# Optimization experiments

Measured on AMD Instinct MI355X. Metric: run time of the kernel, lower is better.

The kernel has to match this reference:

```python
import jax, jax.numpy as jnp
import numpy as np

D_K, D_MODEL, NUM_HEADS = 64, 1024, 16


def _xavier(key, shape):
    # xavier_uniform over last two dims (fan_in=shape[-2], fan_out=shape[-1])
    fan_in, fan_out = shape[-2], shape[-1]
    limit = float(np.sqrt(6.0 / (fan_in + fan_out)))
    return jax.random.uniform(key, shape, jnp.float32, -limit, limit)


def setup_inputs() -> dict:
    key = jax.random.key(0)
    kx, kq, kk, kv, ko = jax.random.split(key, 5)
    x = jax.random.normal(kx, (2, 2048, D_MODEL), dtype=jnp.float32)
    w_q = _xavier(kq, (NUM_HEADS, D_MODEL, D_K))
    w_k = _xavier(kk, (NUM_HEADS, D_MODEL, D_K))
    w_v = _xavier(kv, (NUM_HEADS, D_MODEL, D_K))
    w_o = _xavier(ko, (NUM_HEADS * D_K, D_MODEL))
    return {"x": x, "w_q": w_q, "w_k": w_k, "w_v": w_v, "w_o": w_o}


def reference(x, w_q, w_k, w_v, w_o):
    scale = 1.0 / jnp.sqrt(jnp.asarray(D_K, dtype=jnp.float32))
    q = jnp.einsum('bsd,hdk->bhsk', x, w_q)
    k = jnp.einsum('bsd,hdk->bhsk', x, w_k)
    v = jnp.einsum('bsd,hdk->bhsk', x, w_v)
    scores = jnp.einsum('bhqk,bhmk->bhqm', q, k) * scale  # [B,H,S,S]
    weights = jax.nn.softmax(scores, axis=-1)
    z = jnp.einsum('bhqm,bhmk->bhqk', weights, v)
    b, h, s, dk = z.shape
    z = jnp.transpose(z, (0, 2, 1, 3)).reshape(b, s, h * dk)
    z = jnp.einsum('bse,ed->bsd', z, w_o)
    return x + z  # dropout_prob=0.0 (eval): identity
```

## Files before the change

### kernel.cpp

```cpp
#include <hip/hip_runtime.h>
#include <hip/hip_bf16.h>
#include <stdint.h>

typedef float    f32x4  __attribute__((ext_vector_type(4)));
typedef __bf16   bf16x8 __attribute__((ext_vector_type(8)));
typedef __bf16   bf16x2 __attribute__((ext_vector_type(2)));
typedef uint16_t u16;

#define NHEADS 16
#define DKV    64
#define DMODEL 1024
#define BATCH  2
#define SEQ    2048
#define ROWS   4096

#define EXP2F(x) __builtin_amdgcn_exp2f(x)

__device__ __forceinline__ u16 f2bf(float f) {
  __bf16 h = (__bf16)f;
  union { __bf16 h; u16 u; } c; c.h = h; return c.u;
}
__device__ __forceinline__ uint32_t pk2(float a, float b) {
  union { bf16x2 v; uint32_t u; } c;
  c.v = (bf16x2){(__bf16)a, (__bf16)b};
  return c.u;
}

__device__ __forceinline__ void gload16(const void* g, void* l) {
  __builtin_amdgcn_global_load_lds(
      (const __attribute__((address_space(1))) uint32_t*)g,
      (__attribute__((address_space(3))) uint32_t*)l, 16, 0, 0);
}

__device__ __forceinline__ f32x4 mfma16(bf16x8 a, bf16x8 b, f32x4 c) {
  return __builtin_amdgcn_mfma_f32_16x16x32_bf16(a, b, c, 0, 0, 0);
}

__global__ void prep_kernel(const float* __restrict__ x, u16* __restrict__ xb,
                            const float* __restrict__ wq, const float* __restrict__ wk,
                            const float* __restrict__ wv, const float* __restrict__ wo,
                            u16* __restrict__ wt, u16* __restrict__ wot) {
  int blk = blockIdx.x, tid = threadIdx.x;
  if (blk < 2048) {
    int i = blk * 256 + tid;
    const float4* p = (const float4*)(x + (size_t)i * 8);
    float4 a = p[0], b = p[1];
    uint32_t o0 = pk2(a.x, a.y), o1 = pk2(a.z, a.w);
    uint32_t o2 = pk2(b.x, b.y), o3 = pk2(b.z, b.w);
    uint4 pk = make_uint4(o0, o1, o2, o3);
    *(uint4*)(xb + (size_t)i * 8) = pk;
    return;
  }
  __shared__ float t[64][65];
  int wblk = blk - 2048;
  const float* src; u16* dst; int sld, dld;
  if (wblk < 768) {
    int p = wblk >> 8, rem = wblk & 255;
    int h = rem >> 4, dt = rem & 15;
    const float* w = (p == 0) ? wq : (p == 1) ? wk : wv;
    src = w + ((size_t)h * 1024 + dt * 64) * 64;   sld = 64;
    dst = wt + ((size_t)(p * 1024 + h * 64)) * 1024 + dt * 64; dld = 1024;
  } else {
    int t2 = wblk - 768, rt = t2 >> 4, ct = t2 & 15;
    src = wo + (size_t)(rt * 64) * 1024 + ct * 64;  sld = 1024;
    dst = wot + (size_t)(ct * 64) * 1024 + rt * 64; dld = 1024;
  }
#pragma unroll
  for (int i = 0; i < 16; i++) {
    int e = tid + i * 256, r = e >> 6, c = e & 63;
    t[r][c] = src[(size_t)r * sld + c];
  }
  __syncthreads();
#pragma unroll
  for (int i = 0; i < 16; i++) {
    int e = tid + i * 256, r = e >> 6, c = e & 63;
    dst[(size_t)r * dld + c] = f2bf(t[c][r]);
  }
}

__global__ __launch_bounds__(256) void qkv_gemm(
    const u16* __restrict__ xb, const u16* __restrict__ wt,
    u16* __restrict__ qout, u16* __restrict__ kout, u16* __restrict__ vout) {
  __shared__ __align__(16) u16 As[128 * 64];
  __shared__ __align__(16) u16 Bs[128 * 64];
  int tid = threadIdx.x, l = tid & 63, w = tid >> 6;
  int cpx = gridDim.x >> 3;
  int bid = (blockIdx.x & 7) * cpx + (blockIdx.x >> 3);
  bool vpath = bid >= 512;
  const u16 *A, *Bt; int m0, n0;
  if (!vpath) { A = xb; Bt = wt; m0 = (bid >> 4) * 128; n0 = (bid & 15) * 128; }
  else { int b2 = bid - 512; A = wt + (size_t)2048 * 1024; Bt = xb;
         m0 = (b2 >> 5) * 128; n0 = (b2 & 31) * 128; }
  int wm = (w >> 1) * 64, wn = (w & 1) * 64;
  int cg = l >> 4, cl = l & 15;
  int scb = (l & 7) ^ (l >> 3);
  int swz = (cl & 7) << 4;

  f32x4 acc[4][4];
#pragma unroll
  for (int i = 0; i < 4; i++)
#pragma unroll
    for (int j = 0; j < 4; j++) acc[i][j] = (f32x4){0.f, 0.f, 0.f, 0.f};

  for (int k0 = 0; k0 < 1024; k0 += 64) {
    __syncthreads();
    const u16* ga = A  + (size_t)(m0 + w * 32 + (l >> 3)) * 1024 + k0 + scb * 8;
    const u16* gb = Bt + (size_t)(n0 + w * 32 + (l >> 3)) * 1024 + k0 + scb * 8;
#pragma unroll
    for (int j = 0; j < 4; j++) {
      gload16(ga + (size_t)(j * 8) * 1024, &As[(w * 32 + j * 8) * 64]);
      gload16(gb + (size_t)(j * 8) * 1024, &Bs[(w * 32 + j * 8) * 64]);
    }
    __syncthreads();

    bf16x8 af[4][2], bfr[4][2];
#pragma unroll
    for (int mi = 0; mi < 4; mi++) {
      const char* ap = (const char*)&As[(wm + mi * 16 + cl) * 64];
      af[mi][0] = *(const bf16x8*)(ap + ((cg * 16)      ^ swz));
      af[mi][1] = *(const bf16x8*)(ap + ((64 + cg * 16) ^ swz));
    }
#pragma unroll
    for (int ni = 0; ni < 4; ni++) {
      const char* bp = (const char*)&Bs[(wn + ni * 16 + cl) * 64];
      bfr[ni][0] = *(const bf16x8*)(bp + ((cg * 16)      ^ swz));
      bfr[ni][1] = *(const bf16x8*)(bp + ((64 + cg * 16) ^ swz));
    }
#pragma unroll
    for (int mi = 0; mi < 4; mi++)
#pragma unroll
      for (int ni = 0; ni < 4; ni++) {
        acc[mi][ni] = mfma16(af[mi][0], bfr[ni][0], acc[mi][ni]);
        acc[mi][ni] = mfma16(af[mi][1], bfr[ni][1], acc[mi][ni]);
      }
  }

#pragma unroll
  for (int mi = 0; mi < 4; mi++)
#pragma unroll
    for (int ni = 0; ni < 4; ni++) {
      int nbase = n0 + wn + ni * 16 + cl;
#pragma unroll
      for (int r = 0; r < 4; r++) {
        int m = m0 + wm + mi * 16 + cg * 4 + r;
        float v = acc[mi][ni][r];
        if (!vpath) {
          int p = nbase >> 10, hh = (nbase >> 6) & 15, dk = nbase & 63;
          int b = m >> 11, s = m & 2047;
          size_t o = ((size_t)(b * 16 + hh) * 2048 + s) * 64 + dk;
          if (p == 0) qout[o] = f2bf(v * 0.18033688f);
          else        kout[o] = f2bf(v);
        } else {
          vout[(size_t)m * 4096 + nbase] = f2bf(v);
        }
      }
    }
}

__global__ __launch_bounds__(256) void out_gemm(
    const u16* __restrict__ A, const u16* __restrict__ Bt,
    const float* __restrict__ xres, float* __restrict__ fout) {
  __shared__ __align__(16) u16 As[128 * 64];
  __shared__ __align__(16) u16 Bs[64 * 64];
  int tid = threadIdx.x, l = tid & 63, w = tid >> 6;
  int cpx = gridDim.x >> 3;
  int bid = (blockIdx.x & 7) * cpx + (blockIdx.x >> 3);
  int m0 = (bid >> 4) * 128, n0 = (bid & 15) * 64;
  int wm = (w >> 1) * 64, wn = (w & 1) * 32;
  int cg = l >> 4, cl = l & 15;
  int scb = (l & 7) ^ (l >> 3);
  int swz = (cl & 7) << 4;

  f32x4 acc[4][2];
#pragma unroll
  for (int i = 0; i < 4; i++)
#pragma unroll
    for (int j = 0; j < 2; j++) acc[i][j] = (f32x4){0.f, 0.f, 0.f, 0.f};

  for (int k0 = 0; k0 < 1024; k0 += 64) {
    __syncthreads();
    const u16* ga = A  + (size_t)(m0 + w * 32 + (l >> 3)) * 1024 + k0 + scb * 8;
    const u16* gb = Bt + (size_t)(n0 + w * 16 + (l >> 3)) * 1024 + k0 + scb * 8;
#pragma unroll
    for (int j = 0; j < 4; j++)
      gload16(ga + (size_t)(j * 8) * 1024, &As[(w * 32 + j * 8) * 64]);
#pragma unroll
    for (int j = 0; j < 2; j++)
      gload16(gb + (size_t)(j * 8) * 1024, &Bs[(w * 16 + j * 8) * 64]);
    __syncthreads();

    bf16x8 af[4][2], bfr[2][2];
#pragma unroll
    for (int mi = 0; mi < 4; mi++) {
      const char* ap = (const char*)&As[(wm + mi * 16 + cl) * 64];
      af[mi][0] = *(const bf16x8*)(ap + ((cg * 16)      ^ swz));
      af[mi][1] = *(const bf16x8*)(ap + ((64 + cg * 16) ^ swz));
    }
#pragma unroll
    for (int ni = 0; ni < 2; ni++) {
      const char* bp = (const char*)&Bs[(wn + ni * 16 + cl) * 64];
      bfr[ni][0] = *(const bf16x8*)(bp + ((cg * 16)      ^ swz));
      bfr[ni][1] = *(const bf16x8*)(bp + ((64 + cg * 16) ^ swz));
    }
#pragma unroll
    for (int mi = 0; mi < 4; mi++)
#pragma unroll
      for (int ni = 0; ni < 2; ni++) {
        acc[mi][ni] = mfma16(af[mi][0], bfr[ni][0], acc[mi][ni]);
        acc[mi][ni] = mfma16(af[mi][1], bfr[ni][1], acc[mi][ni]);
      }
  }

#pragma unroll
  for (int mi = 0; mi < 4; mi++)
#pragma unroll
    for (int ni = 0; ni < 2; ni++) {
      int nbase = n0 + wn + ni * 16 + cl;
#pragma unroll
      for (int r = 0; r < 4; r++) {
        int m = m0 + wm + mi * 16 + cg * 4 + r;
        size_t o = (size_t)m * 1024 + nbase;
        fout[o] = acc[mi][ni][r] + xres[o];
      }
    }
}

__global__ __launch_bounds__(256) void attn_kernel(
    const u16* __restrict__ q, const u16* __restrict__ k,
    const u16* __restrict__ vt, u16* __restrict__ z) {
  __shared__ __align__(16) u16 Ks[4][64 * 64];
  __shared__ __align__(16) u16 Vs[4][64 * 64];
  __shared__ __align__(16) u16 Ps[4][32 * 64];
  int tid = threadIdx.x, l = tid & 63, w = tid >> 6;
  int blk = blockIdx.x;
  int xcd = blk & 7, slot0 = blk >> 3;
  int bh = xcd * 4 + (slot0 >> 4), qt = slot0 & 15;
  int b = bh >> 4, h = bh & 15;
  int q0 = qt * 128 + w * 32;
  int cg = l >> 4, cl = l & 15;
  int swz = (cl & 7) << 4;

  const u16* qb = q  + ((size_t)bh * 2048 + q0) * 64;
  const u16* kb = k  + (size_t)bh * 2048 * 64;
  const u16* vb = vt + (size_t)(h * 64) * 4096 + b * 2048;

  int srow = w * 16 + (l >> 3);
  int scb  = (l & 7) ^ (l >> 3);

  bf16x8 bq0[2], bq1[2];
#pragma unroll
  for (int qf = 0; qf < 2; qf++) {
    bq0[qf] = *(const bf16x8*)&qb[(size_t)(qf * 16 + cl) * 64 + cg * 8];
    bq1[qf] = *(const bf16x8*)&qb[(size_t)(qf * 16 + cl) * 64 + 32 + cg * 8];
  }

  f32x4 oacc[2][4];
#pragma unroll
  for (int qf = 0; qf < 2; qf++)
#pragma unroll
    for (int i = 0; i < 4; i++) oacc[qf][i] = (f32x4){0.f, 0.f, 0.f, 0.f};
  float lsum[2] = {0.f, 0.f};

#pragma unroll
  for (int tt = 0; tt < 2; tt++) {
    gload16(kb + ((size_t)tt * 64 + srow) * 64 + scb * 8,       &Ks[tt][(w * 16) * 64]);
    gload16(kb + ((size_t)tt * 64 + srow + 8) * 64 + scb * 8,   &Ks[tt][(w * 16 + 8) * 64]);
    gload16(vb + (size_t)srow * 4096 + tt * 64 + scb * 8,       &Vs[tt][(w * 16) * 64]);
    gload16(vb + (size_t)(srow + 8) * 4096 + tt * 64 + scb * 8, &Vs[tt][(w * 16 + 8) * 64]);
  }
  __syncthreads();

  for (int t = 0; t < 32; t++) {
    int cur = t & 3;
    if (t + 2 < 32) {
      int ns = (t + 2) & 3;
      gload16(kb + ((size_t)(t + 2) * 64 + srow) * 64 + scb * 8,       &Ks[ns][(w * 16) * 64]);
      gload16(kb + ((size_t)(t + 2) * 64 + srow + 8) * 64 + scb * 8,   &Ks[ns][(w * 16 + 8) * 64]);
      gload16(vb + (size_t)srow * 4096 + (t + 2) * 64 + scb * 8,       &Vs[ns][(w * 16) * 64]);
      gload16(vb + (size_t)(srow + 8) * 4096 + (t + 2) * 64 + scb * 8, &Vs[ns][(w * 16 + 8) * 64]);
    }

    f32x4 sc[2][4];
    __builtin_amdgcn_s_setprio(1);
#pragma unroll
    for (int g = 0; g < 4; g++) {
      const char* kp = (const char*)&Ks[cur][(g * 16 + cl) * 64];
      bf16x8 a0 = *(const bf16x8*)(kp + ((cg * 16)      ^ swz));
      bf16x8 a1 = *(const bf16x8*)(kp + ((cg * 16 + 64) ^ swz));
#pragma unroll
      for (int qf = 0; qf < 2; qf++) {
        f32x4 t2 = (f32x4){-16.f, -16.f, -16.f, -16.f};
        t2 = mfma16(a0, bq0[qf], t2);
        t2 = mfma16(a1, bq1[qf], t2);
        sc[qf][g] = t2;
      }
    }
    __builtin_amdgcn_s_setprio(0);

#pragma unroll
    for (int qf = 0; qf < 2; qf++) {
      float rs = 0.f;
#pragma unroll
      for (int g = 0; g < 4; g++)
#pragma unroll
        for (int r = 0; r < 4; r++) {
          float p = EXP2F(sc[qf][g][r]);
          sc[qf][g][r] = p;
          rs += p;
        }
      lsum[qf] += rs;
    }

    bf16x8 pb0[2], pb1[2];
#pragma unroll
    for (int qf = 0; qf < 2; qf++) {
      char* pw = (char*)&Ps[w][(qf * 16 + cl) * 64];
#pragma unroll
      for (int g = 0; g < 4; g++) {
        uint32_t lo = pk2(sc[qf][g][0], sc[qf][g][1]);
        uint32_t hi = pk2(sc[qf][g][2], sc[qf][g][3]);
        *(uint2*)(pw + ((g * 32 + cg * 8) ^ swz)) = make_uint2(lo, hi);
      }
      pb0[qf] = *(const bf16x8*)(pw + ((cg * 16)      ^ swz));
      pb1[qf] = *(const bf16x8*)(pw + ((cg * 16 + 64) ^ swz));
    }

    __builtin_amdgcn_s_setprio(1);
#pragma unroll
    for (int nd = 0; nd < 4; nd++) {
      const char* vp = (const char*)&Vs[cur][(nd * 16 + cl) * 64];
      bf16x8 v0 = *(const bf16x8*)(vp + ((cg * 16)      ^ swz));
      bf16x8 v1 = *(const bf16x8*)(vp + ((cg * 16 + 64) ^ swz));
#pragma unroll
      for (int qf = 0; qf < 2; qf++) {
        oacc[qf][nd] = mfma16(v0, pb0[qf], oacc[qf][nd]);
        oacc[qf][nd] = mfma16(v1, pb1[qf], oacc[qf][nd]);
      }
    }
    __builtin_amdgcn_s_setprio(0);

    if (t & 1) __syncthreads();
  }

#pragma unroll
  for (int qf = 0; qf < 2; qf++) {
    float ls = lsum[qf];
    ls += __shfl_xor(ls, 16);
    ls += __shfl_xor(ls, 32);
    float inv = 1.0f / ls;
    u16* zb = z + ((size_t)(b * 2048) + q0 + qf * 16 + cl) * 1024 + h * 64;
#pragma unroll
    for (int nd = 0; nd < 4; nd++) {
      uint32_t lo = pk2(oacc[qf][nd][0] * inv, oacc[qf][nd][1] * inv);
      uint32_t hi = pk2(oacc[qf][nd][2] * inv, oacc[qf][nd][3] * inv);
      *(uint2*)&zb[nd * 16 + cg * 4] = make_uint2(lo, hi);
    }
  }
}

extern "C" void kernel_launch(void* const* d_in, const int* in_sizes, int n_in,
                              void* d_out, int out_size, void* d_ws, size_t ws_size,
                              hipStream_t stream) {
  const float* x  = (const float*)d_in[0];
  const float* wq = (const float*)d_in[1];
  const float* wk = (const float*)d_in[2];
  const float* wv = (const float*)d_in[3];
  const float* wo = (const float*)d_in[4];
  float* out = (float*)d_out;

  uint8_t* ws = (uint8_t*)d_ws;
  u16* xb  = (u16*)(ws);
  u16* wt  = (u16*)(ws + (8ull  << 20));
  u16* wot = (u16*)(ws + (14ull << 20));
  u16* qb  = (u16*)(ws + (16ull << 20));
  u16* kb  = (u16*)(ws + (24ull << 20));
  u16* vt  = (u16*)(ws + (32ull << 20));
  u16* zb  = (u16*)(ws + (40ull << 20));
  if (ws_size < (48ull << 20)) return;

  prep_kernel<<<3072, 256, 0, stream>>>(x, xb, wq, wk, wv, wo, wt, wot);
  qkv_gemm<<<768, 256, 0, stream>>>(xb, wt, qb, kb, vt);
  attn_kernel<<<512, 256, 0, stream>>>(qb, kb, vt, zb);
  out_gemm<<<512, 256, 0, stream>>>(zb, wot, x, out);
}
```

Baseline: 191.5 us.

## Double-buffer LDS tiles in QKV and output GEMMs to overlap loads with MFMA

Both projection GEMMs now use two LDS buffers per operand. The next K-tile is prefetched with direct global-to-LDS loads while MFMAs run on the current tile, and the two barriers per iteration become one. MFMA sections are also wrapped in s_setprio to favour the compute waves. The cost is doubled LDS use (64KB for qkv_gemm), which may lower occupancy, and the gload16 completion wait before the barrier may limit how much latency is actually hidden.

```diff
diff --git a/kernel.cpp b/kernel.cpp
--- a/kernel.cpp
+++ b/kernel.cpp
@@ -81,8 +81,8 @@
 __global__ __launch_bounds__(256) void qkv_gemm(
     const u16* __restrict__ xb, const u16* __restrict__ wt,
     u16* __restrict__ qout, u16* __restrict__ kout, u16* __restrict__ vout) {
-  __shared__ __align__(16) u16 As[128 * 64];
-  __shared__ __align__(16) u16 Bs[128 * 64];
+  __shared__ __align__(16) u16 As[2][128 * 64];
+  __shared__ __align__(16) u16 Bs[2][128 * 64];
   int tid = threadIdx.x, l = tid & 63, w = tid >> 6;
   int cpx = gridDim.x >> 3;
   int bid = (blockIdx.x & 7) * cpx + (blockIdx.x >> 3);
@@ -95,6 +95,7 @@
   int cg = l >> 4, cl = l & 15;
   int scb = (l & 7) ^ (l >> 3);
   int swz = (cl & 7) << 4;
+  int srow = w * 32 + (l >> 3);
 
   f32x4 acc[4][4];
 #pragma unroll
@@ -102,30 +103,42 @@
 #pragma unroll
     for (int j = 0; j < 4; j++) acc[i][j] = (f32x4){0.f, 0.f, 0.f, 0.f};
 
-  for (int k0 = 0; k0 < 1024; k0 += 64) {
-    __syncthreads();
-    const u16* ga = A  + (size_t)(m0 + w * 32 + (l >> 3)) * 1024 + k0 + scb * 8;
-    const u16* gb = Bt + (size_t)(n0 + w * 32 + (l >> 3)) * 1024 + k0 + scb * 8;
-#pragma unroll
-    for (int j = 0; j < 4; j++) {
-      gload16(ga + (size_t)(j * 8) * 1024, &As[(w * 32 + j * 8) * 64]);
-      gload16(gb + (size_t)(j * 8) * 1024, &Bs[(w * 32 + j * 8) * 64]);
-    }
-    __syncthreads();
+  const u16* ga0 = A  + (size_t)(m0 + srow) * 1024 + scb * 8;
+  const u16* gb0 = Bt + (size_t)(n0 + srow) * 1024 + scb * 8;
+
+#pragma unroll
+  for (int j = 0; j < 4; j++) {
+    gload16(ga0 + (size_t)(j * 8) * 1024, &As[0][(w * 32 + j * 8) * 64]);
+    gload16(gb0 + (size_t)(j * 8) * 1024, &Bs[0][(w * 32 + j * 8) * 64]);
+  }
+  __syncthreads();
+
+  int cur = 0;
+  for (int it = 0; it < 16; ++it) {
+    if (it < 15) {
+      const u16* ga = ga0 + (it + 1) * 64;
+      const u16* gb = gb0 + (it + 1) * 64;
+#pragma unroll
+      for (int j = 0; j < 4; j++) {
+        gload16(ga + (size_t)(j * 8) * 1024, &As[cur ^ 1][(w * 32 + j * 8) * 64]);
+        gload16(gb + (size_t)(j * 8) * 1024, &Bs[cur ^ 1][(w * 32 + j * 8) * 64]);
+      }
+    }
 
     bf16x8 af[4][2], bfr[4][2];
 #pragma unroll
     for (int mi = 0; mi < 4; mi++) {
-      const char* ap = (const char*)&As[(wm + mi * 16 + cl) * 64];
+      const char* ap = (const char*)&As[cur][(wm + mi * 16 + cl) * 64];
       af[mi][0] = *(const bf16x8*)(ap + ((cg * 16)      ^ swz));
       af[mi][1] = *(const bf16x8*)(ap + ((64 + cg * 16) ^ swz));
     }
 #pragma unroll
     for (int ni = 0; ni < 4; ni++) {
-      const char* bp = (const char*)&Bs[(wn + ni * 16 + cl) * 64];
+      const char* bp = (const char*)&Bs[cur][(wn + ni * 16 + cl) * 64];
       bfr[ni][0] = *(const bf16x8*)(bp + ((cg * 16)      ^ swz));
       bfr[ni][1] = *(const bf16x8*)(bp + ((64 + cg * 16) ^ swz));
     }
+    __builtin_amdgcn_s_setprio(1);
 #pragma unroll
     for (int mi = 0; mi < 4; mi++)
 #pragma unroll
@@ -133,6 +146,10 @@
         acc[mi][ni] = mfma16(af[mi][0], bfr[ni][0], acc[mi][ni]);
         acc[mi][ni] = mfma16(af[mi][1], bfr[ni][1], acc[mi][ni]);
       }
+    __builtin_amdgcn_s_setprio(0);
+
+    __syncthreads();
+    cur ^= 1;
   }
 
 #pragma unroll
@@ -160,8 +177,8 @@
 __global__ __launch_bounds__(256) void out_gemm(
     const u16* __restrict__ A, const u16* __restrict__ Bt,
     const float* __restrict__ xres, float* __restrict__ fout) {
-  __shared__ __align__(16) u16 As[128 * 64];
-  __shared__ __align__(16) u16 Bs[64 * 64];
+  __shared__ __align__(16) u16 As[2][128 * 64];
+  __shared__ __align__(16) u16 Bs[2][64 * 64];
   int tid = threadIdx.x, l = tid & 63, w = tid >> 6;
   int cpx = gridDim.x >> 3;
   int bid = (blockIdx.x & 7) * cpx + (blockIdx.x >> 3);
@@ -170,6 +187,8 @@
   int cg = l >> 4, cl = l & 15;
   int scb = (l & 7) ^ (l >> 3);
   int swz = (cl & 7) << 4;
+  int srowA = w * 32 + (l >> 3);
+  int srowB = w * 16 + (l >> 3);
 
   f32x4 acc[4][2];
 #pragma unroll
@@ -177,31 +196,44 @@
 #pragma unroll
     for (int j = 0; j < 2; j++) acc[i][j] = (f32x4){0.f, 0.f, 0.f, 0.f};
 
-  for (int k0 = 0; k0 < 1024; k0 += 64) {
-    __syncthreads();
-    const u16* ga = A  + (size_t)(m0 + w * 32 + (l >> 3)) * 1024 + k0 + scb * 8;
-    const u16* gb = Bt + (size_t)(n0 + w * 16 + (l >> 3)) * 1024 + k0 + scb * 8;
-#pragma unroll
-    for (int j = 0; j < 4; j++)
-      gload16(ga + (size_t)(j * 8) * 1024, &As[(w * 32 + j * 8) * 64]);
-#pragma unroll
-    for (int j = 0; j < 2; j++)
-      gload16(gb + (size_t)(j * 8) * 1024, &Bs[(w * 16 + j * 8) * 64]);
-    __syncthreads();
+  const u16* ga0 = A  + (size_t)(m0 + srowA) * 1024 + scb * 8;
+  const u16* gb0 = Bt + (size_t)(n0 + srowB) * 1024 + scb * 8;
+
+#pragma unroll
+  for (int j = 0; j < 4; j++)
+    gload16(ga0 + (size_t)(j * 8) * 1024, &As[0][(w * 32 + j * 8) * 64]);
+#pragma unroll
+  for (int j = 0; j < 2; j++)
+    gload16(gb0 + (size_t)(j * 8) * 1024, &Bs[0][(w * 16 + j * 8) * 64]);
+  __syncthreads();
+
+  int cur = 0;
+  for (int it = 0; it < 16; ++it) {
+    if (it < 15) {
+      const u16* ga = ga0 + (it + 1) * 64;
+      const u16* gb = gb0 + (it + 1) * 64;
+#pragma unroll
+      for (int j = 0; j < 4; j++)
+        gload16(ga + (size_t)(j * 8) * 1024, &As[cur ^ 1][(w * 32 + j * 8) * 64]);
+#pragma unroll
+      for (int j = 0; j < 2; j++)
+        gload16(gb + (size_t)(j * 8) * 1024, &Bs[cur ^ 1][(w * 16 + j * 8) * 64]);
+    }
 
     bf16x8 af[4][2], bfr[2][2];
 #pragma unroll
     for (int mi = 0; mi < 4; mi++) {
-      const char* ap = (const char*)&As[(wm + mi * 16 + cl) * 64];
+      const char* ap = (const char*)&As[cur][(wm + mi * 16 + cl) * 64];
       af[mi][0] = *(const bf16x8*)(ap + ((cg * 16)      ^ swz));
       af[mi][1] = *(const bf16x8*)(ap + ((64 + cg * 16) ^ swz));
     }
 #pragma unroll
     for (int ni = 0; ni < 2; ni++) {
-      const char* bp = (const char*)&Bs[(wn + ni * 16 + cl) * 64];
+      const char* bp = (const char*)&Bs[cur][(wn + ni * 16 + cl) * 64];
       bfr[ni][0] = *(const bf16x8*)(bp + ((cg * 16)      ^ swz));
       bfr[ni][1] = *(const bf16x8*)(bp + ((64 + cg * 16) ^ swz));
     }
+    __builtin_amdgcn_s_setprio(1);
 #pragma unroll
     for (int mi = 0; mi < 4; mi++)
 #pragma unroll
@@ -209,6 +241,10 @@
         acc[mi][ni] = mfma16(af[mi][0], bfr[ni][0], acc[mi][ni]);
         acc[mi][ni] = mfma16(af[mi][1], bfr[ni][1], acc[mi][ni]);
       }
+    __builtin_amdgcn_s_setprio(0);
+
+    __syncthreads();
+    cur ^= 1;
   }
 
 #pragma unroll
```

New measurement: 191.8 us. Within noise of the previous version (+0.1%).
